# Kernel tuning notes

Measured on AMD Instinct MI355X. Metric: run time of the kernel, lower is better.

The kernel has to match this reference:

```python
import jax, jax.numpy as jnp
import numpy as np

EPS = 1e-5
B, N = 16, 131072

def _bn(x, g, b, m, v):
    # x: [C, N]; inference-mode batchnorm with given stats
    return g[:, None] * (x - m[:, None]) * jax.lax.rsqrt(v[:, None] + EPS) + b[:, None]

def _make_npts():
    base = N // B
    offs = np.linspace(-2048, 2048, B).astype(np.int64)
    npts = np.full(B, base, dtype=np.int64) + offs
    npts[-1] += N - npts.sum()
    assert npts.sum() == N and (npts > 0).all()
    return npts

def setup_inputs() -> dict:
    key = jax.random.key(0)
    ks = jax.random.split(key, 16)
    d = {}
    d["x"] = jax.random.normal(ks[0], (3, N), jnp.float32)
    d["npts"] = jnp.asarray(_make_npts(), jnp.int32)
    def w(k, o, i):
        return jax.random.normal(k, (o, i), jnp.float32) * (1.0 / np.sqrt(i))
    def bnp(k, c):
        k1, k2, k3, k4 = jax.random.split(k, 4)
        return (1.0 + 0.1 * jax.random.normal(k1, (c,), jnp.float32),
                0.1 * jax.random.normal(k2, (c,), jnp.float32),
                0.1 * jax.random.normal(k3, (c,), jnp.float32),
                0.5 + jax.random.uniform(k4, (c,), jnp.float32))
    d["W1"] = w(ks[1], 128, 3);   d["b1"] = jnp.zeros(128, jnp.float32)
    d["g1"], d["be1"], d["m1"], d["v1"] = bnp(ks[2], 128)
    d["W2"] = w(ks[3], 256, 128); d["b2"] = jnp.zeros(256, jnp.float32)
    d["g2"], d["be2"], d["m2"], d["v2"] = bnp(ks[4], 256)
    d["W3"] = w(ks[5], 512, 512); d["b3"] = jnp.zeros(512, jnp.float32)
    d["g3"], d["be3"], d["m3"], d["v3"] = bnp(ks[6], 512)
    d["W4"] = w(ks[7], 1024, 512); d["b4"] = jnp.zeros(1024, jnp.float32)
    d["g4"], d["be4"], d["m4"], d["v4"] = bnp(ks[8], 1024)
    return d

def reference(x, npts,
              W1, b1, g1, be1, m1, v1,
              W2, b2, g2, be2, m2, v2,
              W3, b3, g3, be3, m3, v3,
              W4, b4, g4, be4, m4, v4):
    # segment ids for the ragged point->cloud mapping (replaces torch.split loops)
    seg = jnp.repeat(jnp.arange(B, dtype=jnp.int32), npts, total_repeat_length=N)  # [N]
    h = jax.nn.relu(_bn(W1 @ x + b1[:, None], g1, be1, m1, v1))        # [128, N]
    f = _bn(W2 @ h + b2[:, None], g2, be2, m2, v2)                      # [256, N]
    g = jax.ops.segment_max(f.T, seg, num_segments=B)                   # [B, 256]
    gs = g[seg].T                                                       # [256, N] broadcast back
    xc = jnp.concatenate([gs, f], axis=0)                               # [512, N]
    h3 = jax.nn.relu(_bn(W3 @ xc + b3[:, None], g3, be3, m3, v3))       # [512, N]
    h4 = _bn(W4 @ h3 + b4[:, None], g4, be4, m4, v4)                    # [1024, N]
    v = jax.ops.segment_max(h4.T, seg, num_segments=B)                  # [B, 1024]
    return v
```

## Files before the change

### kernel.cpp

```cpp
#include <hip/hip_runtime.h>
#include <hip/hip_bf16.h>
#include <stdint.h>

#define NTOT 131072
#define NSEG 16
#define EPSV 1e-5f

typedef __attribute__((ext_vector_type(8))) short bf16x8;
typedef __attribute__((ext_vector_type(4))) float f32x4;

struct Args {
  const float* x; const int* npts;
  const float *W1,*b1,*g1,*be1,*m1,*v1;
  const float *W2,*b2,*g2,*be2,*m2,*v2;
  const float *W3,*b3,*g3,*be3,*m3,*v3;
  const float *W4,*b4,*g4,*be4,*m4,*v4;
  int* offs;
  float *a1,*c1,*a2,*c2,*a3,*c3,*a4,*c4;
  unsigned int *gkeys,*vkeys;
  unsigned short *w2b;
  unsigned short *w3p;
  unsigned short *w4p;
  unsigned short *fbufp;
  unsigned short *h3p;
  float* cseg;
  float* out;
};

__device__ inline unsigned int f2key(float f){ unsigned u=__float_as_uint(f); return (u&0x80000000u)? ~u : (u|0x80000000u); }
__device__ inline float key2f(unsigned k){ unsigned u=(k&0x80000000u)? (k^0x80000000u) : ~k; return __uint_as_float(u); }
__device__ inline unsigned short f2bf(float f){ __hip_bfloat16 h=__float2bfloat16(f); return *(unsigned short*)&h; }

__device__ inline void gl16(const void* g, void* l){
  __builtin_amdgcn_global_load_lds((const __attribute__((address_space(1))) unsigned int*)g,
                                   (__attribute__((address_space(3))) unsigned int*)l, 16, 0, 0);
}

__global__ void k_setup(Args A){
  int tid = threadIdx.x;
  if (tid==0){ int s=0; A.offs[0]=0; for (int i=0;i<NSEG;i++){ s+=A.npts[i]; A.offs[i+1]=s; } }
  for (int c=tid;c<128;c+=256){ float a=A.g1[c]*rsqrtf(A.v1[c]+EPSV); A.a1[c]=a; A.c1[c]=A.be1[c]+a*(A.b1[c]-A.m1[c]); }
  for (int c=tid;c<256;c+=256){ float a=A.g2[c]*rsqrtf(A.v2[c]+EPSV); A.a2[c]=a; A.c2[c]=A.be2[c]+a*(A.b2[c]-A.m2[c]); }
  for (int c=tid;c<512;c+=256){ float a=A.g3[c]*rsqrtf(A.v3[c]+EPSV); A.a3[c]=a; A.c3[c]=A.be3[c]+a*(A.b3[c]-A.m3[c]); }
  for (int c=tid;c<1024;c+=256){ float a=A.g4[c]*rsqrtf(A.v4[c]+EPSV); A.a4[c]=a; A.c4[c]=A.be4[c]+a*(A.b4[c]-A.m4[c]); }
  for (int i=tid;i<NSEG*256;i+=256)  A.gkeys[i]=0u;
  for (int i=tid;i<NSEG*1024;i+=256) A.vkeys[i]=0u;
}

__global__ void k_conv(Args A){
  const int n1=256*128;
  const int n2=8*4*512*8;
  const int n3=16*4*1024*8;
  for (int i = blockIdx.x*256+threadIdx.x; i < n1+n2+n3; i += gridDim.x*256){
    if (i<n1) A.w2b[i]=f2bf(A.W2[i]);
    else if (i<n1+n2){
      int o=i-n1; int j=o&7, cout=(o>>3)&511, g=o>>12; int ks=g>>2, kg=g&3;
      A.w3p[o]=f2bf(A.W3[(size_t)cout*512 + 256 + ks*32+kg*8+j]);
    } else {
      int o=i-n1-n2; int j=o&7, cout=(o>>3)&1023, g=o>>13; int ks=g>>2, kg=g&3;
      A.w4p[o]=f2bf(A.W4[(size_t)cout*512 + ks*32+kg*8+j]);
    }
  }
}

__global__ __launch_bounds__(256) void k_l12(Args A){
  __shared__ float w1s[384], a1s[128], c1s[128], a2s[256], c2s[256];
  __shared__ float xs[3][64];
  __shared__ int offs_s[NSEG+1], segp[64];
  __shared__ unsigned short hs[16*64*8];
  int tid=threadIdx.x, pt0=blockIdx.x*64;
  for (int i=tid;i<384;i+=256) w1s[i]=A.W1[i];
  if (tid<128){ a1s[tid]=A.a1[tid]; c1s[tid]=A.c1[tid]; }
  a2s[tid]=A.a2[tid]; c2s[tid]=A.c2[tid];
  if (tid<=NSEG) offs_s[tid]=A.offs[tid];
  if (tid<64){ xs[0][tid]=A.x[pt0+tid]; xs[1][tid]=A.x[NTOT+pt0+tid]; xs[2][tid]=A.x[2*NTOT+pt0+tid]; }
  __syncthreads();
  if (tid<64){ int gp=pt0+tid, s=0; while (gp>=offs_s[s+1]) s++; segp[tid]=s; }
  for (int pair=tid; pair<1024; pair+=256){
    int pt=pair&63, kc=pair>>6;
    float x0=xs[0][pt], x1=xs[1][pt], x2=xs[2][pt];
    unsigned short us[8];
    #pragma unroll
    for (int j=0;j<8;j++){
      int cin=kc*8+j;
      float v = fmaf(w1s[cin*3],x0, fmaf(w1s[cin*3+1],x1, w1s[cin*3+2]*x2));
      v = fmaxf(fmaf(a1s[cin],v,c1s[cin]), 0.f);
      us[j]=f2bf(v);
    }
    uint4 pk;
    pk.x=(unsigned)us[0]|((unsigned)us[1]<<16); pk.y=(unsigned)us[2]|((unsigned)us[3]<<16);
    pk.z=(unsigned)us[4]|((unsigned)us[5]<<16); pk.w=(unsigned)us[6]|((unsigned)us[7]<<16);
    *(uint4*)(&hs[(kc*64+pt)*8]) = pk;
  }
  __syncthreads();
  int lane=tid&63, wv=tid>>6, quad=lane>>4, l16=lane&15;
  int m0=wv*64;
  f32x4 acc[4][4];
  for (int a=0;a<4;a++)
    for (int b=0;b<4;b++)
      acc[a][b]=(f32x4){0.f,0.f,0.f,0.f};
  #pragma unroll
  for (int ks=0; ks<4; ++ks){
    bf16x8 bfr[4];
    #pragma unroll
    for (int nt=0; nt<4; ++nt) bfr[nt]=*(bf16x8*)(&hs[((ks*4+quad)*64 + nt*16 + l16)*8]);
    #pragma unroll
    for (int mt=0; mt<4; ++mt){
      bf16x8 afr = *(const bf16x8*)(&A.w2b[(m0+mt*16+l16)*128 + ks*32 + quad*8]);
      #pragma unroll
      for (int nt=0; nt<4; ++nt)
        acc[mt][nt]=__builtin_amdgcn_mfma_f32_16x16x32_bf16(afr, bfr[nt], acc[mt][nt], 0,0,0);
    }
  }
  bool uni = (segp[0]==segp[63]); int seg0=segp[0];
  size_t tb = (size_t)blockIdx.x*16384;
  #pragma unroll
  for (int mt=0;mt<4;++mt){
    int cout0=m0+mt*16+quad*4;
    int kg=cout0>>3, sub=cout0&7;
    float fv[4][4];
    #pragma unroll
    for (int nt=0;nt<4;++nt)
      #pragma unroll
      for (int r=0;r<4;++r)
        fv[nt][r]=fmaf(a2s[cout0+r], acc[mt][nt][r], c2s[cout0+r]);
    #pragma unroll
    for (int nt=0;nt<4;++nt){
      int ptl=nt*16+l16;
      uint2 pk;
      pk.x=(unsigned)f2bf(fv[nt][0])|((unsigned)f2bf(fv[nt][1])<<16);
      pk.y=(unsigned)f2bf(fv[nt][2])|((unsigned)f2bf(fv[nt][3])<<16);
      *(uint2*)&A.fbufp[tb + (size_t)((kg*64+ptl)*8+sub)] = pk;
    }
    #pragma unroll
    for (int r=0;r<4;++r){
      if (uni){
        float mv=fmaxf(fmaxf(fv[0][r],fv[1][r]),fmaxf(fv[2][r],fv[3][r]));
        #pragma unroll
        for (int off=8;off>=1;off>>=1) mv=fmaxf(mv, __shfl_xor(mv,off));
        if (l16==0) atomicMax(&A.gkeys[seg0*256+cout0+r], f2key(mv));
      } else {
        #pragma unroll
        for (int nt=0;nt<4;++nt)
          atomicMax(&A.gkeys[segp[nt*16+l16]*256+cout0+r], f2key(fv[nt][r]));
      }
    }
  }
}

__global__ void k_cseg(Args A){
  int seg = blockIdx.x>>1; int cout = (blockIdx.x&1)*256 + threadIdx.x;
  __shared__ float gs[256];
  gs[threadIdx.x] = key2f(A.gkeys[seg*256+threadIdx.x]);
  __syncthreads();
  const float* wrow = A.W3 + (size_t)cout*512;
  float s=0.f;
  #pragma unroll 8
  for (int k=0;k<256;k++) s = fmaf(wrow[k], gs[k], s);
  A.cseg[seg*512+cout]=s;
}

__global__ __launch_bounds__(512,2) void k_l3(Args A){
  __shared__ unsigned short wlds[8*4*256*8];
  __shared__ int offs_s[NSEG+1];
  int bid=blockIdx.x; int xcd=bid&7; int j=bid>>3;
  int cgrp=j&1, ptgrp=xcd*64+(j>>1);
  int tid=threadIdx.x, lane=tid&63, wv=tid>>6, quad=lane>>4, l16=lane&15;
  int mq=wv&1, tq=wv>>1;
  for (int i=wv*16;i<wv*16+16;++i){
    int slice=i>>2, q=i&3;
    const char* src=(const char*)(A.w3p + (size_t)slice*4096 + cgrp*2048 + q*512);
    gl16(src + lane*16, (char*)wlds + slice*4096 + q*1024);
  }
  if (tid<=NSEG) offs_s[tid]=A.offs[tid];
  __syncthreads();
  int tg = ptgrp*4 + tq, pt0 = tg*64;
  int sBeg=0; while (pt0 >= offs_s[sBeg+1]) sBeg++;
  int sEnd=sBeg; while (pt0+63 >= offs_s[sEnd+1]) sEnd++;
  bool uni=(sBeg==sEnd);
  int segl[4];
  if (!uni){
    #pragma unroll
    for (int nt=0;nt<4;++nt){ int gp=pt0+nt*16+l16, s=sBeg; while (gp>=offs_s[s+1]) s++; segl[nt]=s; }
  }
  f32x4 acc[8][4];
  for (int a=0;a<8;a++)
    for (int b=0;b<4;b++)
      acc[a][b]=(f32x4){0.f,0.f,0.f,0.f};
  const unsigned short* bsrc = A.fbufp + (size_t)tg*16384;
  bf16x8 bb[2][4];
  #pragma unroll
  for (int nt=0;nt<4;++nt) bb[0][nt]=*(const bf16x8*)(bsrc + (size_t)((quad*64 + nt*16 + l16)*8));
  #pragma unroll
  for (int nt=0;nt<4;++nt) bb[1][nt]=*(const bf16x8*)(bsrc + (size_t)(((4+quad)*64 + nt*16 + l16)*8));
  #pragma unroll
  for (int ksl=0; ksl<8; ++ksl){
    bf16x8 afr[8];
    #pragma unroll
    for (int mt=0;mt<8;++mt) afr[mt]=*(bf16x8*)(&wlds[((ksl*4+quad)*256 + mq*128 + mt*16 + l16)*8]);
    #pragma unroll
    for (int mt=0;mt<8;++mt)
      #pragma unroll
      for (int nt=0;nt<4;++nt)
        acc[mt][nt]=__builtin_amdgcn_mfma_f32_16x16x32_bf16(afr[mt], bb[ksl&1][nt], acc[mt][nt], 0,0,0);
    if (ksl+2<8){
      #pragma unroll
      for (int nt=0;nt<4;++nt) bb[ksl&1][nt]=*(const bf16x8*)(bsrc + (size_t)((((ksl+2)*4+quad)*64 + nt*16 + l16)*8));
    }
  }
  #pragma unroll
  for (int mt=0;mt<8;++mt){
    int cout0=cgrp*256 + mq*128 + mt*16 + quad*4;
    int kg=cout0>>3, sub=cout0&7;
    float sa[4],sc[4],csr[4];
    #pragma unroll
    for (int r=0;r<4;++r){ sa[r]=A.a3[cout0+r]; sc[r]=A.c3[cout0+r]; }
    if (uni){
      #pragma unroll
      for (int r=0;r<4;++r) csr[r]=A.cseg[sBeg*512+cout0+r];
    }
    #pragma unroll
    for (int nt=0;nt<4;++nt){
      int ptl=nt*16+l16;
      unsigned short us[4];
      #pragma unroll
      for (int r=0;r<4;++r){
        float cv = uni? csr[r] : A.cseg[segl[nt]*512+cout0+r];
        float hv = fmaxf(fmaf(sa[r], acc[mt][nt][r]+cv, sc[r]), 0.f);
        us[r]=f2bf(hv);
      }
      uint2 pk;
      pk.x=(unsigned)us[0]|((unsigned)us[1]<<16);
      pk.y=(unsigned)us[2]|((unsigned)us[3]<<16);
      *(uint2*)&A.h3p[(size_t)tg*32768 + (size_t)((kg*64+ptl)*8+sub)] = pk;
    }
  }
}

__global__ __launch_bounds__(512,2) void k_l4(Args A){
  __shared__ unsigned short wlds[16*4*128*8];
  __shared__ int offs_s[NSEG+1];
  int bid=blockIdx.x; int xcd=bid&7; int j=bid>>3;
  int cgrp=j&7, ptgrp=xcd*32+(j>>3);
  int tid=threadIdx.x, lane=tid&63, wv=tid>>6, quad=lane>>4, l16=lane&15;
  for (int i=wv*16;i<wv*16+16;++i){
    int slice=i>>1, half=i&1;
    const char* src=(const char*)(A.w4p + (size_t)slice*8192 + cgrp*1024 + half*512);
    gl16(src + lane*16, (char*)wlds + slice*2048 + half*1024);
  }
  if (tid<=NSEG) offs_s[tid]=A.offs[tid];
  __syncthreads();
  int tg = ptgrp*8 + wv, pt0 = tg*64;
  int sBeg=0; while (pt0 >= offs_s[sBeg+1]) sBeg++;
  int sEnd=sBeg; while (pt0+63 >= offs_s[sEnd+1]) sEnd++;
  bool uni=(sBeg==sEnd);
  int segl[4];
  if (!uni){
    #pragma unroll
    for (int nt=0;nt<4;++nt){ int gp=pt0+nt*16+l16, s=sBeg; while (gp>=offs_s[s+1]) s++; segl[nt]=s; }
  }
  f32x4 acc[8][4];
  for (int a=0;a<8;a++)
    for (int b=0;b<4;b++)
      acc[a][b]=(f32x4){0.f,0.f,0.f,0.f};
  const unsigned short* bsrc = A.h3p + (size_t)tg*32768;
  bf16x8 bb[2][4];
  #pragma unroll
  for (int nt=0;nt<4;++nt) bb[0][nt]=*(const bf16x8*)(bsrc + (size_t)((quad*64 + nt*16 + l16)*8));
  #pragma unroll
  for (int nt=0;nt<4;++nt) bb[1][nt]=*(const bf16x8*)(bsrc + (size_t)(((4+quad)*64 + nt*16 + l16)*8));
  #pragma unroll
  for (int ksl=0; ksl<16; ++ksl){
    bf16x8 afr[8];
    #pragma unroll
    for (int mt=0;mt<8;++mt) afr[mt]=*(bf16x8*)(&wlds[((ksl*4+quad)*128 + mt*16 + l16)*8]);
    #pragma unroll
    for (int mt=0;mt<8;++mt)
      #pragma unroll
      for (int nt=0;nt<4;++nt)
        acc[mt][nt]=__builtin_amdgcn_mfma_f32_16x16x32_bf16(afr[mt], bb[ksl&1][nt], acc[mt][nt], 0,0,0);
    if (ksl+2<16){
      #pragma unroll
      for (int nt=0;nt<4;++nt) bb[ksl&1][nt]=*(const bf16x8*)(bsrc + (size_t)((((ksl+2)*4+quad)*64 + nt*16 + l16)*8));
    }
  }
  #pragma unroll
  for (int mt=0;mt<8;++mt){
    int cout0=cgrp*128 + mt*16 + quad*4;
    #pragma unroll
    for (int r=0;r<4;++r){
      int cout=cout0+r;
      float sa=A.a4[cout], sc=A.c4[cout];
      float mv=-3.4e38f;
      #pragma unroll
      for (int nt=0;nt<4;++nt){
        float fv=fmaf(sa, acc[mt][nt][r], sc);
        if (uni) mv=fmaxf(mv,fv);
        else atomicMax(&A.vkeys[segl[nt]*1024+cout], f2key(fv));
      }
      if (uni){
        #pragma unroll
        for (int off=8;off>=1;off>>=1) mv=fmaxf(mv, __shfl_xor(mv,off));
        if (l16==0) atomicMax(&A.vkeys[sBeg*1024+cout], f2key(mv));
      }
    }
  }
}

__global__ void k_final(Args A){
  int i=blockIdx.x*256+threadIdx.x;
  if (i<NSEG*1024) A.out[i]=key2f(A.vkeys[i]);
}

extern "C" void kernel_launch(void* const* d_in, const int* in_sizes, int n_in,
                              void* d_out, int out_size, void* d_ws, size_t ws_size,
                              hipStream_t stream){
  Args A;
  A.x  =(const float*)d_in[0];  A.npts=(const int*)d_in[1];
  A.W1 =(const float*)d_in[2];  A.b1 =(const float*)d_in[3];
  A.g1 =(const float*)d_in[4];  A.be1=(const float*)d_in[5];
  A.m1 =(const float*)d_in[6];  A.v1 =(const float*)d_in[7];
  A.W2 =(const float*)d_in[8];  A.b2 =(const float*)d_in[9];
  A.g2 =(const float*)d_in[10]; A.be2=(const float*)d_in[11];
  A.m2 =(const float*)d_in[12]; A.v2 =(const float*)d_in[13];
  A.W3 =(const float*)d_in[14]; A.b3 =(const float*)d_in[15];
  A.g3 =(const float*)d_in[16]; A.be3=(const float*)d_in[17];
  A.m3 =(const float*)d_in[18]; A.v3 =(const float*)d_in[19];
  A.W4 =(const float*)d_in[20]; A.b4 =(const float*)d_in[21];
  A.g4 =(const float*)d_in[22]; A.be4=(const float*)d_in[23];
  A.m4 =(const float*)d_in[24]; A.v4 =(const float*)d_in[25];

  char* w=(char*)d_ws;
  auto alloc=[&](size_t b)->void*{ void* p=(void*)w; w += (b+255)&~(size_t)255; return p; };
  A.offs =(int*)alloc((NSEG+1)*4);
  A.a1=(float*)alloc(128*4);  A.c1=(float*)alloc(128*4);
  A.a2=(float*)alloc(256*4);  A.c2=(float*)alloc(256*4);
  A.a3=(float*)alloc(512*4);  A.c3=(float*)alloc(512*4);
  A.a4=(float*)alloc(1024*4); A.c4=(float*)alloc(1024*4);
  A.gkeys=(unsigned int*)alloc(NSEG*256*4);
  A.vkeys=(unsigned int*)alloc(NSEG*1024*4);
  A.cseg =(float*)alloc(NSEG*512*4);
  A.w2b=(unsigned short*)alloc(256*128*2);
  A.w3p=(unsigned short*)alloc(131072*2);
  A.w4p=(unsigned short*)alloc(524288*2);
  A.fbufp=(unsigned short*)alloc((size_t)2048*16384*2);
  A.h3p  =(unsigned short*)alloc((size_t)2048*32768*2);
  A.out=(float*)d_out;

  k_setup<<<dim3(1),dim3(256),0,stream>>>(A);
  k_conv <<<dim3(2688),dim3(256),0,stream>>>(A);
  k_l12  <<<dim3(NTOT/64),dim3(256),0,stream>>>(A);
  k_cseg <<<dim3(32),dim3(256),0,stream>>>(A);
  k_l3   <<<dim3(1024),dim3(512),0,stream>>>(A);
  k_l4   <<<dim3(2048),dim3(512),0,stream>>>(A);
  k_final<<<dim3(64),dim3(256),0,stream>>>(A);
}
```

Before: 681.4 us.

## Stream weights and activations through a 4-buffer LDS pipeline in L3/L4 GEMMs

Reorganizes packed weight and activation buffers into 256-point by 256-channel tiles with K-slices laid out contiguously. k_l3 and k_l4 now stage both the A (weights) and B (activations) K-slices into LDS with async global_load_lds. A 4-deep ring buffer is synchronized by explicit vmcnt waits and barriers, replacing direct global loads of B and a full up-front weight preload. The block tile in k_l4 changes to 256 channels x 256 points, and s_setprio wraps the MFMA bursts. This is meant to improve data reuse and hide load latency, at the cost of hand-tuned waitcnt logic and a per-K-slice barrier.

```diff
diff --git a/kernel.cpp b/kernel.cpp
--- a/kernel.cpp
+++ b/kernel.cpp
@@ -49,16 +49,16 @@
 
 __global__ void k_conv(Args A){
   const int n1=256*128;
-  const int n2=8*4*512*8;
-  const int n3=16*4*1024*8;
+  const int n2=131072;
+  const int n3=524288;
   for (int i = blockIdx.x*256+threadIdx.x; i < n1+n2+n3; i += gridDim.x*256){
     if (i<n1) A.w2b[i]=f2bf(A.W2[i]);
     else if (i<n1+n2){
-      int o=i-n1; int j=o&7, cout=(o>>3)&511, g=o>>12; int ks=g>>2, kg=g&3;
-      A.w3p[o]=f2bf(A.W3[(size_t)cout*512 + 256 + ks*32+kg*8+j]);
+      int o=i-n1; int j=o&7, cout=(o>>3)&255, kgrel=(o>>11)&3, ks=(o>>13)&7, cg=(o>>16)&1;
+      A.w3p[o]=f2bf(A.W3[(size_t)(cg*256+cout)*512 + 256 + ks*32 + kgrel*8 + j]);
     } else {
-      int o=i-n1-n2; int j=o&7, cout=(o>>3)&1023, g=o>>13; int ks=g>>2, kg=g&3;
-      A.w4p[o]=f2bf(A.W4[(size_t)cout*512 + ks*32+kg*8+j]);
+      int o=i-n1-n2; int j=o&7, cout=(o>>3)&255, kgrel=(o>>11)&3, ks=(o>>13)&15, cg=(o>>17)&3;
+      A.w4p[o]=f2bf(A.W4[(size_t)(cg*256+cout)*512 + ks*32 + kgrel*8 + j]);
     }
   }
 }
@@ -113,7 +113,8 @@
     }
   }
   bool uni = (segp[0]==segp[63]); int seg0=segp[0];
-  size_t tb = (size_t)blockIdx.x*16384;
+  size_t tb = (size_t)(blockIdx.x>>2)*65536;
+  int prelb = (blockIdx.x&3)*64;
   #pragma unroll
   for (int mt=0;mt<4;++mt){
     int cout0=m0+mt*16+quad*4;
@@ -130,7 +131,7 @@
       uint2 pk;
       pk.x=(unsigned)f2bf(fv[nt][0])|((unsigned)f2bf(fv[nt][1])<<16);
       pk.y=(unsigned)f2bf(fv[nt][2])|((unsigned)f2bf(fv[nt][3])<<16);
-      *(uint2*)&A.fbufp[tb + (size_t)((kg*64+ptl)*8+sub)] = pk;
+      *(uint2*)&A.fbufp[tb + (size_t)((kg*256 + prelb + ptl)*8 + sub)] = pk;
     }
     #pragma unroll
     for (int r=0;r<4;++r){
@@ -161,53 +162,76 @@
 }
 
 __global__ __launch_bounds__(512,2) void k_l3(Args A){
-  __shared__ unsigned short wlds[8*4*256*8];
+  __shared__ unsigned short sA[4][8192];
+  __shared__ unsigned short sB[4][8192];
   __shared__ int offs_s[NSEG+1];
-  int bid=blockIdx.x; int xcd=bid&7; int j=bid>>3;
-  int cgrp=j&1, ptgrp=xcd*64+(j>>1);
+  const int NS=8;
+  int bid=blockIdx.x, xcd=bid&7, j=bid>>3;
+  int cgrp=j&1, ptblk=xcd*64+(j>>1);
   int tid=threadIdx.x, lane=tid&63, wv=tid>>6, quad=lane>>4, l16=lane&15;
   int mq=wv&1, tq=wv>>1;
-  for (int i=wv*16;i<wv*16+16;++i){
-    int slice=i>>2, q=i&3;
-    const char* src=(const char*)(A.w3p + (size_t)slice*4096 + cgrp*2048 + q*512);
-    gl16(src + lane*16, (char*)wlds + slice*4096 + q*1024);
-  }
+  const char* wbase0 = (const char*)A.w3p + (size_t)cgrp*131072;
+  const char* bbase0 = (const char*)A.fbufp + (size_t)ptblk*131072;
   if (tid<=NSEG) offs_s[tid]=A.offs[tid];
-  __syncthreads();
-  int tg = ptgrp*4 + tq, pt0 = tg*64;
+
+  auto stage=[&](int buf, int s){
+    char* lA=(char*)&sA[buf][0];
+    char* lB=(char*)&sB[buf][0];
+    if (wv<4){
+      const char* src = wbase0 + (size_t)s*16384;
+      #pragma unroll
+      for (int i=0;i<4;++i){ int c=wv*4+i; gl16(src + c*1024 + lane*16, lA + c*1024); }
+    } else {
+      const char* src = bbase0 + (size_t)s*16384;
+      #pragma unroll
+      for (int i=0;i<4;++i){ int c=(wv-4)*4+i; gl16(src + c*1024 + lane*16, lB + c*1024); }
+    }
+  };
+
+  f32x4 acc[8][4];
+  for (int a=0;a<8;a++)
+    for (int b=0;b<4;b++)
+      acc[a][b]=(f32x4){0.f,0.f,0.f,0.f};
+
+  stage(0,0); stage(1,1);
+  asm volatile("s_waitcnt lgkmcnt(0)" ::: "memory");
+  asm volatile("s_waitcnt vmcnt(4)" ::: "memory");
+  __builtin_amdgcn_s_barrier();
+  __builtin_amdgcn_sched_barrier(0);
+
+  #pragma unroll
+  for (int s=0;s<NS;++s){
+    int cur=s&3;
+    if (s+2<NS) stage((s+2)&3, s+2);
+    if (s+2<NS)      asm volatile("s_waitcnt vmcnt(8)" ::: "memory");
+    else if (s+1<NS) asm volatile("s_waitcnt vmcnt(4)" ::: "memory");
+    else             asm volatile("s_waitcnt vmcnt(0)" ::: "memory");
+    __builtin_amdgcn_s_barrier();
+    __builtin_amdgcn_sched_barrier(0);
+    bf16x8 afr[8], bb[4];
+    #pragma unroll
+    for (int mt=0;mt<8;++mt) afr[mt]=*(const bf16x8*)(&sA[cur][(quad*256 + mq*128 + mt*16 + l16)*8]);
+    #pragma unroll
+    for (int nt=0;nt<4;++nt) bb[nt]=*(const bf16x8*)(&sB[cur][(quad*256 + tq*64 + nt*16 + l16)*8]);
+    __builtin_amdgcn_s_setprio(1);
+    #pragma unroll
+    for (int mt=0;mt<8;++mt)
+      #pragma unroll
+      for (int nt=0;nt<4;++nt)
+        acc[mt][nt]=__builtin_amdgcn_mfma_f32_16x16x32_bf16(afr[mt], bb[nt], acc[mt][nt], 0,0,0);
+    __builtin_amdgcn_s_setprio(0);
+  }
+
+  int pt0 = ptblk*256 + tq*64;
   int sBeg=0; while (pt0 >= offs_s[sBeg+1]) sBeg++;
   int sEnd=sBeg; while (pt0+63 >= offs_s[sEnd+1]) sEnd++;
   bool uni=(sBeg==sEnd);
   int segl[4];
   if (!uni){
     #pragma unroll
-    for (int nt=0;nt<4;++nt){ int gp=pt0+nt*16+l16, s=sBeg; while (gp>=offs_s[s+1]) s++; segl[nt]=s; }
-  }
-  f32x4 acc[8][4];
-  for (int a=0;a<8;a++)
-    for (int b=0;b<4;b++)
-      acc[a][b]=(f32x4){0.f,0.f,0.f,0.f};
-  const unsigned short* bsrc = A.fbufp + (size_t)tg*16384;
-  bf16x8 bb[2][4];
-  #pragma unroll
-  for (int nt=0;nt<4;++nt) bb[0][nt]=*(const bf16x8*)(bsrc + (size_t)((quad*64 + nt*16 + l16)*8));
-  #pragma unroll
-  for (int nt=0;nt<4;++nt) bb[1][nt]=*(const bf16x8*)(bsrc + (size_t)(((4+quad)*64 + nt*16 + l16)*8));
-  #pragma unroll
-  for (int ksl=0; ksl<8; ++ksl){
-    bf16x8 afr[8];
-    #pragma unroll
-    for (int mt=0;mt<8;++mt) afr[mt]=*(bf16x8*)(&wlds[((ksl*4+quad)*256 + mq*128 + mt*16 + l16)*8]);
-    #pragma unroll
-    for (int mt=0;mt<8;++mt)
-      #pragma unroll
-      for (int nt=0;nt<4;++nt)
-        acc[mt][nt]=__builtin_amdgcn_mfma_f32_16x16x32_bf16(afr[mt], bb[ksl&1][nt], acc[mt][nt], 0,0,0);
-    if (ksl+2<8){
-      #pragma unroll
-      for (int nt=0;nt<4;++nt) bb[ksl&1][nt]=*(const bf16x8*)(bsrc + (size_t)((((ksl+2)*4+quad)*64 + nt*16 + l16)*8));
-    }
-  }
+    for (int nt=0;nt<4;++nt){ int gp=pt0+nt*16+l16, ss=sBeg; while (gp>=offs_s[ss+1]) ss++; segl[nt]=ss; }
+  }
+  size_t hb = (size_t)ptblk*131072;
   #pragma unroll
   for (int mt=0;mt<8;++mt){
     int cout0=cgrp*256 + mq*128 + mt*16 + quad*4;
@@ -221,7 +245,7 @@
     }
     #pragma unroll
     for (int nt=0;nt<4;++nt){
-      int ptl=nt*16+l16;
+      int prel=tq*64+nt*16+l16;
       unsigned short us[4];
       #pragma unroll
       for (int r=0;r<4;++r){
@@ -232,61 +256,84 @@
       uint2 pk;
       pk.x=(unsigned)us[0]|((unsigned)us[1]<<16);
       pk.y=(unsigned)us[2]|((unsigned)us[3]<<16);
-      *(uint2*)&A.h3p[(size_t)tg*32768 + (size_t)((kg*64+ptl)*8+sub)] = pk;
+      *(uint2*)&A.h3p[hb + (size_t)((kg*256+prel)*8+sub)] = pk;
     }
   }
 }
 
 __global__ __launch_bounds__(512,2) void k_l4(Args A){
-  __shared__ unsigned short wlds[16*4*128*8];
+  __shared__ unsigned short sA[4][8192];
+  __shared__ unsigned short sB[4][8192];
   __shared__ int offs_s[NSEG+1];
-  int bid=blockIdx.x; int xcd=bid&7; int j=bid>>3;
-  int cgrp=j&7, ptgrp=xcd*32+(j>>3);
+  const int NS=16;
+  int bid=blockIdx.x, xcd=bid&7, j=bid>>3;
+  int cgrp=j&3, ptblk=xcd*64+(j>>2);
   int tid=threadIdx.x, lane=tid&63, wv=tid>>6, quad=lane>>4, l16=lane&15;
-  for (int i=wv*16;i<wv*16+16;++i){
-    int slice=i>>1, half=i&1;
-    const char* src=(const char*)(A.w4p + (size_t)slice*8192 + cgrp*1024 + half*512);
-    gl16(src + lane*16, (char*)wlds + slice*2048 + half*1024);
-  }
+  int mq=wv&1, tq=wv>>1;
+  const char* wbase0 = (const char*)A.w4p + (size_t)cgrp*262144;
+  const char* bbase0 = (const char*)A.h3p + (size_t)ptblk*262144;
   if (tid<=NSEG) offs_s[tid]=A.offs[tid];
-  __syncthreads();
-  int tg = ptgrp*8 + wv, pt0 = tg*64;
+
+  auto stage=[&](int buf, int s){
+    char* lA=(char*)&sA[buf][0];
+    char* lB=(char*)&sB[buf][0];
+    if (wv<4){
+      const char* src = wbase0 + (size_t)s*16384;
+      #pragma unroll
+      for (int i=0;i<4;++i){ int c=wv*4+i; gl16(src + c*1024 + lane*16, lA + c*1024); }
+    } else {
+      const char* src = bbase0 + (size_t)s*16384;
+      #pragma unroll
+      for (int i=0;i<4;++i){ int c=(wv-4)*4+i; gl16(src + c*1024 + lane*16, lB + c*1024); }
+    }
+  };
+
+  f32x4 acc[8][4];
+  for (int a=0;a<8;a++)
+    for (int b=0;b<4;b++)
+      acc[a][b]=(f32x4){0.f,0.f,0.f,0.f};
+
+  stage(0,0); stage(1,1);
+  asm volatile("s_waitcnt lgkmcnt(0)" ::: "memory");
+  asm volatile("s_waitcnt vmcnt(4)" ::: "memory");
+  __builtin_amdgcn_s_barrier();
+  __builtin_amdgcn_sched_barrier(0);
+
+  #pragma unroll
+  for (int s=0;s<NS;++s){
+    int cur=s&3;
+    if (s+2<NS) stage((s+2)&3, s+2);
+    if (s+2<NS)      asm volatile("s_waitcnt vmcnt(8)" ::: "memory");
+    else if (s+1<NS) asm volatile("s_waitcnt vmcnt(4)" ::: "memory");
+    else             asm volatile("s_waitcnt vmcnt(0)" ::: "memory");
+    __builtin_amdgcn_s_barrier();
+    __builtin_amdgcn_sched_barrier(0);
+    bf16x8 afr[8], bb[4];
+    #pragma unroll
+    for (int mt=0;mt<8;++mt) afr[mt]=*(const bf16x8*)(&sA[cur][(quad*256 + mq*128 + mt*16 + l16)*8]);
+    #pragma unroll
+    for (int nt=0;nt<4;++nt) bb[nt]=*(const bf16x8*)(&sB[cur][(quad*256 + tq*64 + nt*16 + l16)*8]);
+    __builtin_amdgcn_s_setprio(1);
+    #pragma unroll
+    for (int mt=0;mt<8;++mt)
+      #pragma unroll
+      for (int nt=0;nt<4;++nt)
+        acc[mt][nt]=__builtin_amdgcn_mfma_f32_16x16x32_bf16(afr[mt], bb[nt], acc[mt][nt], 0,0,0);
+    __builtin_amdgcn_s_setprio(0);
+  }
+
+  int pt0 = ptblk*256 + tq*64;
   int sBeg=0; while (pt0 >= offs_s[sBeg+1]) sBeg++;
   int sEnd=sBeg; while (pt0+63 >= offs_s[sEnd+1]) sEnd++;
   bool uni=(sBeg==sEnd);
   int segl[4];
   if (!uni){
     #pragma unroll
-    for (int nt=0;nt<4;++nt){ int gp=pt0+nt*16+l16, s=sBeg; while (gp>=offs_s[s+1]) s++; segl[nt]=s; }
-  }
-  f32x4 acc[8][4];
-  for (int a=0;a<8;a++)
-    for (int b=0;b<4;b++)
-      acc[a][b]=(f32x4){0.f,0.f,0.f,0.f};
-  const unsigned short* bsrc = A.h3p + (size_t)tg*32768;
-  bf16x8 bb[2][4];
-  #pragma unroll
-  for (int nt=0;nt<4;++nt) bb[0][nt]=*(const bf16x8*)(bsrc + (size_t)((quad*64 + nt*16 + l16)*8));
-  #pragma unroll
-  for (int nt=0;nt<4;++nt) bb[1][nt]=*(const bf16x8*)(bsrc + (size_t)(((4+quad)*64 + nt*16 + l16)*8));
-  #pragma unroll
-  for (int ksl=0; ksl<16; ++ksl){
-    bf16x8 afr[8];
-    #pragma unroll
-    for (int mt=0;mt<8;++mt) afr[mt]=*(bf16x8*)(&wlds[((ksl*4+quad)*128 + mt*16 + l16)*8]);
-    #pragma unroll
-    for (int mt=0;mt<8;++mt)
-      #pragma unroll
-      for (int nt=0;nt<4;++nt)
-        acc[mt][nt]=__builtin_amdgcn_mfma_f32_16x16x32_bf16(afr[mt], bb[ksl&1][nt], acc[mt][nt], 0,0,0);
-    if (ksl+2<16){
-      #pragma unroll
-      for (int nt=0;nt<4;++nt) bb[ksl&1][nt]=*(const bf16x8*)(bsrc + (size_t)((((ksl+2)*4+quad)*64 + nt*16 + l16)*8));
-    }
+    for (int nt=0;nt<4;++nt){ int gp=pt0+nt*16+l16, ss=sBeg; while (gp>=offs_s[ss+1]) ss++; segl[nt]=ss; }
   }
   #pragma unroll
   for (int mt=0;mt<8;++mt){
-    int cout0=cgrp*128 + mt*16 + quad*4;
+    int cout0=cgrp*256 + mq*128 + mt*16 + quad*4;
     #pragma unroll
     for (int r=0;r<4;++r){
       int cout=cout0+r;
@@ -343,8 +390,8 @@
   A.w2b=(unsigned short*)alloc(256*128*2);
   A.w3p=(unsigned short*)alloc(131072*2);
   A.w4p=(unsigned short*)alloc(524288*2);
-  A.fbufp=(unsigned short*)alloc((size_t)2048*16384*2);
-  A.h3p  =(unsigned short*)alloc((size_t)2048*32768*2);
+  A.fbufp=(unsigned short*)alloc((size_t)512*65536*2);
+  A.h3p  =(unsigned short*)alloc((size_t)512*131072*2);
   A.out=(float*)d_out;
 
   k_setup<<<dim3(1),dim3(256),0,stream>>>(A);
```

New measurement: 728.3 us. +6.9%, slower.

## Retile layer-3/4 GEMMs as 128x128 tiles with LDS-staged A and B

Applied to the files above, without the earlier changes.

Replaces the layer-3 and layer-4 kernels, which held a whole weight slab in LDS and streamed activations from global into registers per wave, with a classic 128x128 tiled GEMM. Each 256-thread block stages both weight and activation K-slices into LDS through global_load_lds, with one sync pair per slice. Weight packing and the f/h3 intermediate layouts are changed to 128-point, 128-channel tiles to match. This trades the prior single weight load per block for more, smaller blocks with higher occupancy and shared activation reuse, but adds per-slice barriers with no double buffering.

```diff
diff --git a/kernel.cpp b/kernel.cpp
--- a/kernel.cpp
+++ b/kernel.cpp
@@ -49,16 +49,16 @@
 
 __global__ void k_conv(Args A){
   const int n1=256*128;
-  const int n2=8*4*512*8;
-  const int n3=16*4*1024*8;
+  const int n2=131072;
+  const int n3=524288;
   for (int i = blockIdx.x*256+threadIdx.x; i < n1+n2+n3; i += gridDim.x*256){
     if (i<n1) A.w2b[i]=f2bf(A.W2[i]);
     else if (i<n1+n2){
-      int o=i-n1; int j=o&7, cout=(o>>3)&511, g=o>>12; int ks=g>>2, kg=g&3;
-      A.w3p[o]=f2bf(A.W3[(size_t)cout*512 + 256 + ks*32+kg*8+j]);
+      int o=i-n1; int j=o&7, cr=(o>>3)&127, kgg=(o>>10)&31, mt=o>>15;
+      A.w3p[o]=f2bf(A.W3[(size_t)(mt*128+cr)*512 + 256 + kgg*8 + j]);
     } else {
-      int o=i-n1-n2; int j=o&7, cout=(o>>3)&1023, g=o>>13; int ks=g>>2, kg=g&3;
-      A.w4p[o]=f2bf(A.W4[(size_t)cout*512 + ks*32+kg*8+j]);
+      int o=i-n1-n2; int j=o&7, cr=(o>>3)&127, kgg=(o>>10)&63, mt=o>>16;
+      A.w4p[o]=f2bf(A.W4[(size_t)(mt*128+cr)*512 + kgg*8 + j]);
     }
   }
 }
@@ -113,7 +113,8 @@
     }
   }
   bool uni = (segp[0]==segp[63]); int seg0=segp[0];
-  size_t tb = (size_t)blockIdx.x*16384;
+  size_t tb = (size_t)(blockIdx.x>>1)*32768;
+  int prelb = (blockIdx.x&1)*64;
   #pragma unroll
   for (int mt=0;mt<4;++mt){
     int cout0=m0+mt*16+quad*4;
@@ -130,7 +131,7 @@
       uint2 pk;
       pk.x=(unsigned)f2bf(fv[nt][0])|((unsigned)f2bf(fv[nt][1])<<16);
       pk.y=(unsigned)f2bf(fv[nt][2])|((unsigned)f2bf(fv[nt][3])<<16);
-      *(uint2*)&A.fbufp[tb + (size_t)((kg*64+ptl)*8+sub)] = pk;
+      *(uint2*)&A.fbufp[tb + (size_t)((kg*128 + prelb + ptl)*8 + sub)] = pk;
     }
     #pragma unroll
     for (int r=0;r<4;++r){
@@ -160,57 +161,57 @@
   A.cseg[seg*512+cout]=s;
 }
 
-__global__ __launch_bounds__(512,2) void k_l3(Args A){
-  __shared__ unsigned short wlds[8*4*256*8];
+__global__ __launch_bounds__(256,4) void k_l3(Args A){
+  __shared__ unsigned short sA[8192], sB[8192];
   __shared__ int offs_s[NSEG+1];
-  int bid=blockIdx.x; int xcd=bid&7; int j=bid>>3;
-  int cgrp=j&1, ptgrp=xcd*64+(j>>1);
+  int bid=blockIdx.x, xcd=bid&7, idx=bid>>3;
+  int mtile=idx&3, ntile=xcd*128+(idx>>2);
   int tid=threadIdx.x, lane=tid&63, wv=tid>>6, quad=lane>>4, l16=lane&15;
-  int mq=wv&1, tq=wv>>1;
-  for (int i=wv*16;i<wv*16+16;++i){
-    int slice=i>>2, q=i&3;
-    const char* src=(const char*)(A.w3p + (size_t)slice*4096 + cgrp*2048 + q*512);
-    gl16(src + lane*16, (char*)wlds + slice*4096 + q*1024);
-  }
+  int mq=wv&1, nq=wv>>1;
+  const char* wbase=(const char*)A.w3p   + (size_t)mtile*65536;
+  const char* bbase=(const char*)A.fbufp + (size_t)ntile*65536;
   if (tid<=NSEG) offs_s[tid]=A.offs[tid];
-  __syncthreads();
-  int tg = ptgrp*4 + tq, pt0 = tg*64;
+  f32x4 acc[4][4];
+  for (int a=0;a<4;a++)
+    for (int b=0;b<4;b++)
+      acc[a][b]=(f32x4){0.f,0.f,0.f,0.f};
+  for (int s=0;s<4;++s){
+    const char* srcA = wbase + s*16384;
+    const char* srcB = bbase + s*16384;
+    #pragma unroll
+    for (int i=0;i<4;++i){
+      gl16(srcA + wv*4096 + i*1024 + lane*16, (char*)sA + wv*4096 + i*1024);
+      gl16(srcB + wv*4096 + i*1024 + lane*16, (char*)sB + wv*4096 + i*1024);
+    }
+    __syncthreads();
+    #pragma unroll
+    for (int ks=0;ks<2;++ks){
+      bf16x8 bb[4], afr[4];
+      #pragma unroll
+      for (int nt=0;nt<4;++nt) bb[nt]=*(const bf16x8*)(&sB[((ks*4+quad)*128 + nq*64 + nt*16 + l16)*8]);
+      #pragma unroll
+      for (int mt=0;mt<4;++mt) afr[mt]=*(const bf16x8*)(&sA[((ks*4+quad)*128 + mq*64 + mt*16 + l16)*8]);
+      #pragma unroll
+      for (int mt=0;mt<4;++mt)
+        #pragma unroll
+        for (int nt=0;nt<4;++nt)
+          acc[mt][nt]=__builtin_amdgcn_mfma_f32_16x16x32_bf16(afr[mt], bb[nt], acc[mt][nt], 0,0,0);
+    }
+    __syncthreads();
+  }
+  int pt0 = ntile*128 + nq*64;
   int sBeg=0; while (pt0 >= offs_s[sBeg+1]) sBeg++;
   int sEnd=sBeg; while (pt0+63 >= offs_s[sEnd+1]) sEnd++;
   bool uni=(sBeg==sEnd);
   int segl[4];
   if (!uni){
     #pragma unroll
-    for (int nt=0;nt<4;++nt){ int gp=pt0+nt*16+l16, s=sBeg; while (gp>=offs_s[s+1]) s++; segl[nt]=s; }
-  }
-  f32x4 acc[8][4];
-  for (int a=0;a<8;a++)
-    for (int b=0;b<4;b++)
-      acc[a][b]=(f32x4){0.f,0.f,0.f,0.f};
-  const unsigned short* bsrc = A.fbufp + (size_t)tg*16384;
-  bf16x8 bb[2][4];
+    for (int nt=0;nt<4;++nt){ int gp=pt0+nt*16+l16, ss=sBeg; while (gp>=offs_s[ss+1]) ss++; segl[nt]=ss; }
+  }
+  size_t hb = (size_t)ntile*65536;
   #pragma unroll
-  for (int nt=0;nt<4;++nt) bb[0][nt]=*(const bf16x8*)(bsrc + (size_t)((quad*64 + nt*16 + l16)*8));
-  #pragma unroll
-  for (int nt=0;nt<4;++nt) bb[1][nt]=*(const bf16x8*)(bsrc + (size_t)(((4+quad)*64 + nt*16 + l16)*8));
-  #pragma unroll
-  for (int ksl=0; ksl<8; ++ksl){
-    bf16x8 afr[8];
-    #pragma unroll
-    for (int mt=0;mt<8;++mt) afr[mt]=*(bf16x8*)(&wlds[((ksl*4+quad)*256 + mq*128 + mt*16 + l16)*8]);
-    #pragma unroll
-    for (int mt=0;mt<8;++mt)
-      #pragma unroll
-      for (int nt=0;nt<4;++nt)
-        acc[mt][nt]=__builtin_amdgcn_mfma_f32_16x16x32_bf16(afr[mt], bb[ksl&1][nt], acc[mt][nt], 0,0,0);
-    if (ksl+2<8){
-      #pragma unroll
-      for (int nt=0;nt<4;++nt) bb[ksl&1][nt]=*(const bf16x8*)(bsrc + (size_t)((((ksl+2)*4+quad)*64 + nt*16 + l16)*8));
-    }
-  }
-  #pragma unroll
-  for (int mt=0;mt<8;++mt){
-    int cout0=cgrp*256 + mq*128 + mt*16 + quad*4;
+  for (int mt=0;mt<4;++mt){
+    int cout0=mtile*128 + mq*64 + mt*16 + quad*4;
     int kg=cout0>>3, sub=cout0&7;
     float sa[4],sc[4],csr[4];
     #pragma unroll
@@ -221,7 +222,7 @@
     }
     #pragma unroll
     for (int nt=0;nt<4;++nt){
-      int ptl=nt*16+l16;
+      int prel=nq*64+nt*16+l16;
       unsigned short us[4];
       #pragma unroll
       for (int r=0;r<4;++r){
@@ -232,61 +233,61 @@
       uint2 pk;
       pk.x=(unsigned)us[0]|((unsigned)us[1]<<16);
       pk.y=(unsigned)us[2]|((unsigned)us[3]<<16);
-      *(uint2*)&A.h3p[(size_t)tg*32768 + (size_t)((kg*64+ptl)*8+sub)] = pk;
-    }
-  }
-}
-
-__global__ __launch_bounds__(512,2) void k_l4(Args A){
-  __shared__ unsigned short wlds[16*4*128*8];
+      *(uint2*)&A.h3p[hb + (size_t)((kg*128+prel)*8+sub)] = pk;
+    }
+  }
+}
+
+__global__ __launch_bounds__(256,4) void k_l4(Args A){
+  __shared__ unsigned short sA[8192], sB[8192];
   __shared__ int offs_s[NSEG+1];
-  int bid=blockIdx.x; int xcd=bid&7; int j=bid>>3;
-  int cgrp=j&7, ptgrp=xcd*32+(j>>3);
+  int bid=blockIdx.x, xcd=bid&7, idx=bid>>3;
+  int mtile=idx&7, ntile=xcd*128+(idx>>3);
   int tid=threadIdx.x, lane=tid&63, wv=tid>>6, quad=lane>>4, l16=lane&15;
-  for (int i=wv*16;i<wv*16+16;++i){
-    int slice=i>>1, half=i&1;
-    const char* src=(const char*)(A.w4p + (size_t)slice*8192 + cgrp*1024 + half*512);
-    gl16(src + lane*16, (char*)wlds + slice*2048 + half*1024);
-  }
+  int mq=wv&1, nq=wv>>1;
+  const char* wbase=(const char*)A.w4p + (size_t)mtile*131072;
+  const char* bbase=(const char*)A.h3p + (size_t)ntile*131072;
   if (tid<=NSEG) offs_s[tid]=A.offs[tid];
-  __syncthreads();
-  int tg = ptgrp*8 + wv, pt0 = tg*64;
+  f32x4 acc[4][4];
+  for (int a=0;a<4;a++)
+    for (int b=0;b<4;b++)
+      acc[a][b]=(f32x4){0.f,0.f,0.f,0.f};
+  for (int s=0;s<8;++s){
+    const char* srcA = wbase + s*16384;
+    const char* srcB = bbase + s*16384;
+    #pragma unroll
+    for (int i=0;i<4;++i){
+      gl16(srcA + wv*4096 + i*1024 + lane*16, (char*)sA + wv*4096 + i*1024);
+      gl16(srcB + wv*4096 + i*1024 + lane*16, (char*)sB + wv*4096 + i*1024);
+    }
+    __syncthreads();
+    #pragma unroll
+    for (int ks=0;ks<2;++ks){
+      bf16x8 bb[4], afr[4];
+      #pragma unroll
+      for (int nt=0;nt<4;++nt) bb[nt]=*(const bf16x8*)(&sB[((ks*4+quad)*128 + nq*64 + nt*16 + l16)*8]);
+      #pragma unroll
+      for (int mt=0;mt<4;++mt) afr[mt]=*(const bf16x8*)(&sA[((ks*4+quad)*128 + mq*64 + mt*16 + l16)*8]);
+      #pragma unroll
+      for (int mt=0;mt<4;++mt)
+        #pragma unroll
+        for (int nt=0;nt<4;++nt)
+          acc[mt][nt]=__builtin_amdgcn_mfma_f32_16x16x32_bf16(afr[mt], bb[nt], acc[mt][nt], 0,0,0);
+    }
+    __syncthreads();
+  }
+  int pt0 = ntile*128 + nq*64;
   int sBeg=0; while (pt0 >= offs_s[sBeg+1]) sBeg++;
   int sEnd=sBeg; while (pt0+63 >= offs_s[sEnd+1]) sEnd++;
   bool uni=(sBeg==sEnd);
   int segl[4];
   if (!uni){
     #pragma unroll
-    for (int nt=0;nt<4;++nt){ int gp=pt0+nt*16+l16, s=sBeg; while (gp>=offs_s[s+1]) s++; segl[nt]=s; }
-  }
-  f32x4 acc[8][4];
-  for (int a=0;a<8;a++)
-    for (int b=0;b<4;b++)
-      acc[a][b]=(f32x4){0.f,0.f,0.f,0.f};
-  const unsigned short* bsrc = A.h3p + (size_t)tg*32768;
-  bf16x8 bb[2][4];
+    for (int nt=0;nt<4;++nt){ int gp=pt0+nt*16+l16, ss=sBeg; while (gp>=offs_s[ss+1]) ss++; segl[nt]=ss; }
+  }
   #pragma unroll
-  for (int nt=0;nt<4;++nt) bb[0][nt]=*(const bf16x8*)(bsrc + (size_t)((quad*64 + nt*16 + l16)*8));
-  #pragma unroll
-  for (int nt=0;nt<4;++nt) bb[1][nt]=*(const bf16x8*)(bsrc + (size_t)(((4+quad)*64 + nt*16 + l16)*8));
-  #pragma unroll
-  for (int ksl=0; ksl<16; ++ksl){
-    bf16x8 afr[8];
-    #pragma unroll
-    for (int mt=0;mt<8;++mt) afr[mt]=*(bf16x8*)(&wlds[((ksl*4+quad)*128 + mt*16 + l16)*8]);
-    #pragma unroll
-    for (int mt=0;mt<8;++mt)
-      #pragma unroll
-      for (int nt=0;nt<4;++nt)
-        acc[mt][nt]=__builtin_amdgcn_mfma_f32_16x16x32_bf16(afr[mt], bb[ksl&1][nt], acc[mt][nt], 0,0,0);
-    if (ksl+2<16){
-      #pragma unroll
-      for (int nt=0;nt<4;++nt) bb[ksl&1][nt]=*(const bf16x8*)(bsrc + (size_t)((((ksl+2)*4+quad)*64 + nt*16 + l16)*8));
-    }
-  }
-  #pragma unroll
-  for (int mt=0;mt<8;++mt){
-    int cout0=cgrp*128 + mt*16 + quad*4;
+  for (int mt=0;mt<4;++mt){
+    int cout0=mtile*128 + mq*64 + mt*16 + quad*4;
     #pragma unroll
     for (int r=0;r<4;++r){
       int cout=cout0+r;
@@ -343,15 +344,15 @@
   A.w2b=(unsigned short*)alloc(256*128*2);
   A.w3p=(unsigned short*)alloc(131072*2);
   A.w4p=(unsigned short*)alloc(524288*2);
-  A.fbufp=(unsigned short*)alloc((size_t)2048*16384*2);
-  A.h3p  =(unsigned short*)alloc((size_t)2048*32768*2);
+  A.fbufp=(unsigned short*)alloc((size_t)1024*32768*2);
+  A.h3p  =(unsigned short*)alloc((size_t)1024*65536*2);
   A.out=(float*)d_out;
 
   k_setup<<<dim3(1),dim3(256),0,stream>>>(A);
   k_conv <<<dim3(2688),dim3(256),0,stream>>>(A);
   k_l12  <<<dim3(NTOT/64),dim3(256),0,stream>>>(A);
   k_cseg <<<dim3(32),dim3(256),0,stream>>>(A);
-  k_l3   <<<dim3(1024),dim3(512),0,stream>>>(A);
-  k_l4   <<<dim3(2048),dim3(512),0,stream>>>(A);
+  k_l3   <<<dim3(4096),dim3(256),0,stream>>>(A);
+  k_l4   <<<dim3(8192),dim3(256),0,stream>>>(A);
   k_final<<<dim3(64),dim3(256),0,stream>>>(A);
 }
```

Measured after the change: 604.2 us. 1.13x faster.
